# Kernel tuning notes

Measured on AMD Instinct MI355X. Metric: run time of the kernel, lower is better.

The kernel has to match this reference:

```python
import jax, jax.numpy as jnp
import numpy as np

N = 50000
IN_C = 128
HID = 128  # 2 * out_channels
OUT_C = 64
E = 800000


def setup_inputs() -> dict:
    key = jax.random.key(0)
    k1, k2, k3, k4, k5, k6 = jax.random.split(key, 6)
    x = jax.random.normal(k1, (N, IN_C), dtype=jnp.float32)
    edge_index = jax.random.randint(k2, (2, E), 0, N, dtype=jnp.int64)
    # Glorot init like PyG GCNConv
    W1 = jax.random.normal(k3, (IN_C, HID), dtype=jnp.float32) * np.sqrt(2.0 / (IN_C + HID))
    b1 = jnp.zeros((HID,), dtype=jnp.float32)
    W2 = jax.random.normal(k4, (HID, OUT_C), dtype=jnp.float32) * np.sqrt(2.0 / (HID + OUT_C))
    b2 = jnp.zeros((OUT_C,), dtype=jnp.float32)
    return {"x": x, "edge_index": edge_index, "W1": W1, "b1": b1, "W2": W2, "b2": b2}


def _gcn_norm(edge_index, num_nodes):
    # PyG gcn_norm with add_self_loops=True, edge_weight=1:
    # deg[i] = number of incoming edges to i (including self loop)
    # norm(e) = deg[src]^-0.5 * deg[dst]^-0.5
    loops = jnp.arange(num_nodes, dtype=edge_index.dtype)
    src = jnp.concatenate([edge_index[0], loops])
    dst = jnp.concatenate([edge_index[1], loops])
    deg = jax.ops.segment_sum(jnp.ones_like(dst, dtype=jnp.float32), dst,
                              num_segments=num_nodes)
    dinv = jnp.where(deg > 0, jax.lax.rsqrt(deg), 0.0)
    norm = dinv[src] * dinv[dst]
    return src, dst, norm


def _gcn_layer(x, W, b, src, dst, norm, num_nodes):
    h = x @ W                                    # [N, D_out] dense GEMM first (PyG order)
    msg = h[src] * norm[:, None]                 # gather + scale: [E+N, D_out]
    out = jax.ops.segment_sum(msg, dst, num_segments=num_nodes)  # scatter-add
    return out + b


def reference(x, edge_index, W1, b1, W2, b2):
    num_nodes = x.shape[0]
    # cached=True in the original: normalization computed once, reused by both convs
    src, dst, norm = _gcn_norm(edge_index, num_nodes)
    h = _gcn_layer(x, W1, b1, src, dst, norm, num_nodes)
    h = jax.nn.relu(h)
    out = _gcn_layer(h, W2, b2, src, dst, norm, num_nodes)
    return out
```

## Files before the change

### kernel.cpp

```cpp
#include <hip/hip_runtime.h>
#include <hip/hip_bf16.h>


typedef unsigned short ushort_t;
typedef __attribute__((ext_vector_type(8))) short bf16x8;
typedef __attribute__((ext_vector_type(4))) float f32x4;

__device__ __forceinline__ float blo(int v) {
    union { int i; float f; } u;
    u.i = v << 16;
    return u.f;
}

__device__ __forceinline__ float bhi(int v) {
    union { int i; float f; } u;
    u.i = v & 0xffff0000;
    return u.f;
}

__device__ __forceinline__ ushort_t f2bf(float f) {
    __hip_bfloat16 h = __float2bfloat16(f);
    return *reinterpret_cast<ushort_t*>(&h);
}

#define BMAX 512
#define CHUNK 2048
#define CAP 3072


__global__ __launch_bounds__(256) void gemm1bin_k(const float* __restrict__ X,
                                                  const float* __restrict__ W,
                                                  ushort_t* __restrict__ H,
                                                  const int* __restrict__ src,
                                                  const int* __restrict__ dst,
                                                  int* __restrict__ bucket_cursor,
                                                  int* __restrict__ binned,
                                                  int n, int E, int G1) {
    __shared__ __align__(16) char smem[52224];
    const int t = threadIdx.x;

    if ((int)blockIdx.x < G1) {
        ushort_t (*As)[136] = reinterpret_cast<ushort_t(*)[136]>(smem);
        ushort_t (*Bt)[136] = reinterpret_cast<ushort_t(*)[136]>(smem + 64 * 136 * 2);
        const int row0 = blockIdx.x * 64;
#pragma unroll
        for (int rep = 0; rep < 8; rep++) {
            int idx = rep * 1024 + t * 4;
            int r = idx >> 7, c = idx & 127;
            int gr = row0 + r;
            float4 v = make_float4(0.f, 0.f, 0.f, 0.f);
            if (gr < n) v = *reinterpret_cast<const float4*>(X + (size_t)gr * 128 + c);
            As[r][c + 0] = f2bf(v.x); As[r][c + 1] = f2bf(v.y);
            As[r][c + 2] = f2bf(v.z); As[r][c + 3] = f2bf(v.w);
        }
#pragma unroll
        for (int rep = 0; rep < 16; rep++) {
            int idx = rep * 1024 + t * 4;
            int k = idx >> 7, nn = idx & 127;
            float4 v = *reinterpret_cast<const float4*>(W + k * 128 + nn);
            Bt[nn + 0][k] = f2bf(v.x); Bt[nn + 1][k] = f2bf(v.y);
            Bt[nn + 2][k] = f2bf(v.z); Bt[nn + 3][k] = f2bf(v.w);
        }
        __syncthreads();
        const int lane = t & 63;
        const int wave = t >> 6;
        const int l15 = lane & 15;
        const int koff = (lane >> 4) * 8;
        f32x4 acc[8] = {};
#pragma unroll
        for (int ks = 0; ks < 4; ks++) {
            int kb = ks * 32 + koff;
            bf16x8 a = *reinterpret_cast<const bf16x8*>(&As[wave * 16 + l15][kb]);
#pragma unroll
            for (int tc = 0; tc < 8; tc++) {
                bf16x8 b = *reinterpret_cast<const bf16x8*>(&Bt[tc * 16 + l15][kb]);
                acc[tc] = __builtin_amdgcn_mfma_f32_16x16x32_bf16(a, b, acc[tc], 0, 0, 0);
            }
        }
        const int rbase = row0 + wave * 16 + (lane >> 4) * 4;
#pragma unroll
        for (int reg = 0; reg < 4; reg++) {
            int gr = rbase + reg;
            if (gr < n) {
#pragma unroll
                for (int tc = 0; tc < 8; tc++)
                    H[(size_t)gr * 128 + tc * 16 + l15] = f2bf(acc[tc][reg]);
            }
        }
    } else {
        int* lcnt = (int*)smem;
        int* lbase = lcnt + BMAX;
        int* lcur = lbase + BMAX;
        const int nchunks = (E + CHUNK - 1) / CHUNK;
        const int nbin = (int)gridDim.x - G1;
        for (int ch = (int)blockIdx.x - G1; ch < nchunks; ch += nbin) {
            int base = ch * CHUNK;
            int cnt = min(CHUNK, E - base);
            for (int i = t; i < BMAX; i += 256) lcnt[i] = 0;
            __syncthreads();
            for (int k = t; k < cnt; k += 256)
                atomicAdd(&lcnt[dst[base + k] >> 7], 1);
            __syncthreads();
            for (int i = t; i < BMAX; i += 256) {
                int c = lcnt[i];
                if (c) lbase[i] = atomicAdd(&bucket_cursor[i], c);
                lcur[i] = 0;
            }
            __syncthreads();
            for (int k = t; k < cnt; k += 256) {
                int d = dst[base + k];
                int b = d >> 7;
                int r = atomicAdd(&lcur[b], 1);
                int pos = lbase[b] + r;
                if (pos < CAP)
                    binned[b * CAP + pos] = (src[base + k] << 7) | (d & 127);
            }
            __syncthreads();
        }
    }
}

__global__ __launch_bounds__(256) void finalize_k(const int* __restrict__ binned,
                                                  const int* __restrict__ bucket_cursor,
                                                  float* __restrict__ dinv,
                                                  int2* __restrict__ row_range,
                                                  ushort_t* __restrict__ csr,
                                                  int N, int B) {
    __shared__ int dcnt[128];
    __shared__ int ebase[128];
    __shared__ int sc[128];
    int b = blockIdx.x;
    int tid = threadIdx.x;
    int node0 = b << 7;
    int nn = min(128, N - node0);
    int e0 = b * CAP;
    int e1 = e0 + min(bucket_cursor[b], CAP);

    if (tid < 128) dcnt[tid] = 0;
    __syncthreads();
    for (int k = e0 + tid; k < e1; k += 256)
        atomicAdd(&dcnt[binned[k] & 127], 1);
    __syncthreads();
    if (tid < 128) sc[tid] = (tid < nn) ? dcnt[tid] : 0;
    __syncthreads();
    for (int off = 1; off < 128; off <<= 1) {
        int t = 0;
        if (tid < 128 && tid >= off) t = sc[tid - off];
        __syncthreads();
        if (tid < 128) sc[tid] += t;
        __syncthreads();
    }
    if (tid < nn) {
        int deg = dcnt[tid];
        int ex = sc[tid] - deg;
        ebase[tid] = ex;
        int g = node0 + tid;
        dinv[g] = rsqrtf((float)deg + 1.0f);
        row_range[g] = make_int2(e0 + ex, e0 + ex + deg);
        dcnt[tid] = 0;
    }
    __syncthreads();
    const int t1 = N / 3, t2 = 2 * (N / 3);
#pragma unroll
    for (int ph = 0; ph < 3; ph++) {
        int lo = (ph == 0) ? 0 : (ph == 1 ? t1 : t2);
        int hi = (ph == 0) ? t1 : (ph == 1 ? t2 : N);
        for (int k = e0 + tid; k < e1; k += 256) {
            int e = binned[k];
            int s = (int)((unsigned)e >> 7);
            if (s >= lo && s < hi) {
                int low = e & 127;
                int r = atomicAdd(&dcnt[low], 1);
                csr[e0 + ebase[low] + r] = (ushort_t)s;
            }
        }
        __syncthreads();
    }
}


__global__ __launch_bounds__(256) void gemm2_k(const ushort_t* __restrict__ X,
                                               const float* __restrict__ W,
                                               const float* __restrict__ dinv,
                                               ushort_t* __restrict__ H, int n) {
    __shared__ ushort_t As[64][136];
    __shared__ ushort_t Bt[64][136];
    const int t = threadIdx.x;
    const int row0 = blockIdx.x * 64;
#pragma unroll
    for (int rep = 0; rep < 8; rep++) {
        int idx = rep * 1024 + t * 4;
        int r = idx >> 7, c = idx & 127;
        int gr = row0 + r;
        ushort4 v = make_ushort4(0, 0, 0, 0);
        if (gr < n) v = *reinterpret_cast<const ushort4*>(X + (size_t)gr * 128 + c);
        As[r][c + 0] = v.x; As[r][c + 1] = v.y; As[r][c + 2] = v.z; As[r][c + 3] = v.w;
    }
#pragma unroll
    for (int rep = 0; rep < 8; rep++) {
        int idx = rep * 1024 + t * 4;
        int k = idx >> 6, nn = idx & 63;
        float4 v = *reinterpret_cast<const float4*>(W + k * 64 + nn);
        Bt[nn + 0][k] = f2bf(v.x); Bt[nn + 1][k] = f2bf(v.y);
        Bt[nn + 2][k] = f2bf(v.z); Bt[nn + 3][k] = f2bf(v.w);
    }
    __syncthreads();
    const int lane = t & 63;
    const int wave = t >> 6;
    const int l15 = lane & 15;
    const int koff = (lane >> 4) * 8;
    f32x4 acc[4] = {};
#pragma unroll
    for (int ks = 0; ks < 4; ks++) {
        int kb = ks * 32 + koff;
        bf16x8 a = *reinterpret_cast<const bf16x8*>(&As[wave * 16 + l15][kb]);
#pragma unroll
        for (int tc = 0; tc < 4; tc++) {
            bf16x8 b = *reinterpret_cast<const bf16x8*>(&Bt[tc * 16 + l15][kb]);
            acc[tc] = __builtin_amdgcn_mfma_f32_16x16x32_bf16(a, b, acc[tc], 0, 0, 0);
        }
    }
    const int rbase = row0 + wave * 16 + (lane >> 4) * 4;
#pragma unroll
    for (int reg = 0; reg < 4; reg++) {
        int gr = rbase + reg;
        if (gr < n) {
            float dv = dinv[gr];
#pragma unroll
            for (int tc = 0; tc < 4; tc++)
                H[(size_t)gr * 64 + tc * 16 + l15] = f2bf(acc[tc][reg] * dv);
        }
    }
}

#define FMA8(VV, WT)                                                    \
    a0 = fmaf(blo((VV).x), (WT), a0); a1 = fmaf(bhi((VV).x), (WT), a1); \
    a2 = fmaf(blo((VV).y), (WT), a2); a3 = fmaf(bhi((VV).y), (WT), a3); \
    a4 = fmaf(blo((VV).z), (WT), a4); a5 = fmaf(bhi((VV).z), (WT), a5); \
    a6 = fmaf(blo((VV).w), (WT), a6); a7 = fmaf(bhi((VV).w), (WT), a7);


__global__ __launch_bounds__(256) void agg1_k(const ushort_t* __restrict__ h,
                                              const int2* __restrict__ row_range,
                                              const ushort_t* __restrict__ csr,
                                              const float* __restrict__ dinv,
                                              const float* __restrict__ bias,
                                              ushort_t* __restrict__ out, int n) {
    const int t = threadIdx.x;
    const int i = blockIdx.x * 16 + (t >> 4);
    if (i >= n) return;
    const int q = t & 15;
    const ushort_t* hq = h + 8 * q;
    float a0 = 0.f, a1 = 0.f, a2 = 0.f, a3 = 0.f;
    float a4 = 0.f, a5 = 0.f, a6 = 0.f, a7 = 0.f;
    const int2 rr = row_range[i];
    const int e = rr.y - 1;
    for (int j = rr.x; j < rr.y; j += 8) {
#pragma unroll
        for (int k = 0; k < 8; k++) {
            int jk = min(j + k, e);
            int s = (int)csr[jk];
            float w = (j + k <= e) ? dinv[s] : 0.f;
            int4 v = *reinterpret_cast<const int4*>(hq + (size_t)s * 128);
            FMA8(v, w);
        }
    }
    const float di = dinv[i];
    int4 sv = *reinterpret_cast<const int4*>(hq + (size_t)i * 128);
    FMA8(sv, di);
    float4 b0 = *reinterpret_cast<const float4*>(bias + 8 * q);
    float4 b1v = *reinterpret_cast<const float4*>(bias + 8 * q + 4);
    int4 o;
    o.x = (int)(((unsigned)f2bf(fmaxf(fmaf(di, a1, b0.y), 0.f)) << 16) | f2bf(fmaxf(fmaf(di, a0, b0.x), 0.f)));
    o.y = (int)(((unsigned)f2bf(fmaxf(fmaf(di, a3, b0.w), 0.f)) << 16) | f2bf(fmaxf(fmaf(di, a2, b0.z), 0.f)));
    o.z = (int)(((unsigned)f2bf(fmaxf(fmaf(di, a5, b1v.y), 0.f)) << 16) | f2bf(fmaxf(fmaf(di, a4, b1v.x), 0.f)));
    o.w = (int)(((unsigned)f2bf(fmaxf(fmaf(di, a7, b1v.w), 0.f)) << 16) | f2bf(fmaxf(fmaf(di, a6, b1v.z), 0.f)));
    *reinterpret_cast<int4*>(out + (size_t)i * 128 + 8 * q) = o;
}


__global__ __launch_bounds__(256) void agg2_k(const ushort_t* __restrict__ h,
                                              const int2* __restrict__ row_range,
                                              const ushort_t* __restrict__ csr,
                                              const float* __restrict__ dinv,
                                              const float* __restrict__ bias,
                                              float* __restrict__ out, int n) {
    const int t = threadIdx.x;
    const int i = blockIdx.x * 32 + (t >> 3);
    if (i >= n) return;
    const int q = t & 7;
    const ushort_t* hq = h + 8 * q;
    float a0 = 0.f, a1 = 0.f, a2 = 0.f, a3 = 0.f;
    float a4 = 0.f, a5 = 0.f, a6 = 0.f, a7 = 0.f;
    const int2 rr = row_range[i];
    const int e = rr.y - 1;
    for (int j = rr.x; j < rr.y; j += 8) {
#pragma unroll
        for (int k = 0; k < 8; k++) {
            int jk = min(j + k, e);
            int s = (int)csr[jk];
            float w = (j + k <= e) ? 1.f : 0.f;
            int4 v = *reinterpret_cast<const int4*>(hq + (size_t)s * 64);
            FMA8(v, w);
        }
    }
    int4 sv = *reinterpret_cast<const int4*>(hq + (size_t)i * 64);
    FMA8(sv, 1.f);
    const float di = dinv[i];
    float4 b0 = *reinterpret_cast<const float4*>(bias + 8 * q);
    float4 b1v = *reinterpret_cast<const float4*>(bias + 8 * q + 4);
    float4 o0 = make_float4(fmaf(di, a0, b0.x), fmaf(di, a1, b0.y),
                            fmaf(di, a2, b0.z), fmaf(di, a3, b0.w));
    float4 o1 = make_float4(fmaf(di, a4, b1v.x), fmaf(di, a5, b1v.y),
                            fmaf(di, a6, b1v.z), fmaf(di, a7, b1v.w));
    *reinterpret_cast<float4*>(out + (size_t)i * 64 + 8 * q) = o0;
    *reinterpret_cast<float4*>(out + (size_t)i * 64 + 8 * q + 4) = o1;
}


extern "C" void kernel_launch(void* const* d_in, const int* in_sizes, int n_in,
                              void* d_out, int out_size, void* d_ws, size_t ws_size,
                              hipStream_t stream) {
    const float* x   = (const float*)d_in[0];
    const int*   ei  = (const int*)d_in[1];
    const float* W1  = (const float*)d_in[2];
    const float* b1  = (const float*)d_in[3];
    const float* W2  = (const float*)d_in[4];
    const float* b2  = (const float*)d_in[5];
    float* out = (float*)d_out;

    const int N = in_sizes[0] / 128;
    const int E = in_sizes[1] / 2;
    const int B = (N + 127) >> 7;
    const int* src = ei;
    const int* dst = ei + E;

    char* p = (char*)d_ws;
    auto alloc = [&](size_t bytes) {
        char* q = p;
        p += (bytes + 255) & ~(size_t)255;
        return (void*)q;
    };
    int*      bucket_cursor = (int*)alloc((size_t)BMAX * 4);
    float*    dinv          = (float*)alloc((size_t)N * 4);
    int2*     row_range     = (int2*)alloc((size_t)N * 8);
    int*      binned        = (int*)alloc((size_t)B * CAP * 4);
    ushort_t* csr           = (ushort_t*)alloc(((size_t)B * CAP + 32) * 2);
    ushort_t* h1            = (ushort_t*)alloc((size_t)N * 128 * 2);
    ushort_t* agg1          = (ushort_t*)alloc((size_t)N * 128 * 2);
    ushort_t* h2            = h1;

    const int nchunks = (E + CHUNK - 1) / CHUNK;
    const int G1 = (N + 63) / 64;

    (void)hipMemsetAsync(bucket_cursor, 0, (size_t)B * 4, stream);
    gemm1bin_k<<<G1 + nchunks, 256, 0, stream>>>(x, W1, h1, src, dst,
                                                 bucket_cursor, binned, N, E, G1);
    finalize_k<<<B, 256, 0, stream>>>(binned, bucket_cursor, dinv, row_range, csr, N, B);

    agg1_k<<<(N + 15) / 16, 256, 0, stream>>>(h1, row_range, csr, dinv, b1, agg1, N);

    gemm2_k<<<(N + 63) / 64, 256, 0, stream>>>(agg1, W2, dinv, h2, N);
    agg2_k<<<(N + 31) / 32, 256, 0, stream>>>(h2, row_range, csr, dinv, b2, out, N);
}
```

Measured before the change: 185.4 us.

## Fuse layer-1 aggregation with layer-2 GEMM and split CSR fill into more phases

Layer-1 aggregation now writes its ReLU'd bf16 rows for each block of 16 nodes into shared memory, and the same block multiplies them by W2 with MFMA. This removes the separate gemm2 kernel and the global round trip of the N×128 intermediate. The cost is that every block re-converts all of W2 into shared memory, and the larger shared-memory footprint may lower occupancy. The finalize kernel's source-range phases go from 3 to 8, which changes the CSR fill ordering and locality but adds more passes over the binned edges.

```diff
diff --git a/kernel.cpp b/kernel.cpp
--- a/kernel.cpp
+++ b/kernel.cpp
@@ -26,6 +26,7 @@
 #define BMAX 512
 #define CHUNK 2048
 #define CAP 3072
+#define NPH 8
 
 
 __global__ __launch_bounds__(256) void gemm1bin_k(const float* __restrict__ X,
@@ -160,11 +161,10 @@
         dcnt[tid] = 0;
     }
     __syncthreads();
-    const int t1 = N / 3, t2 = 2 * (N / 3);
-#pragma unroll
-    for (int ph = 0; ph < 3; ph++) {
-        int lo = (ph == 0) ? 0 : (ph == 1 ? t1 : t2);
-        int hi = (ph == 0) ? t1 : (ph == 1 ? t2 : N);
+#pragma unroll
+    for (int ph = 0; ph < NPH; ph++) {
+        int lo = (int)((long long)N * ph / NPH);
+        int hi = (int)((long long)N * (ph + 1) / NPH);
         for (int k = e0 + tid; k < e1; k += 256) {
             int e = binned[k];
             int s = (int)((unsigned)e >> 7);
@@ -178,61 +178,6 @@
     }
 }
 
-
-__global__ __launch_bounds__(256) void gemm2_k(const ushort_t* __restrict__ X,
-                                               const float* __restrict__ W,
-                                               const float* __restrict__ dinv,
-                                               ushort_t* __restrict__ H, int n) {
-    __shared__ ushort_t As[64][136];
-    __shared__ ushort_t Bt[64][136];
-    const int t = threadIdx.x;
-    const int row0 = blockIdx.x * 64;
-#pragma unroll
-    for (int rep = 0; rep < 8; rep++) {
-        int idx = rep * 1024 + t * 4;
-        int r = idx >> 7, c = idx & 127;
-        int gr = row0 + r;
-        ushort4 v = make_ushort4(0, 0, 0, 0);
-        if (gr < n) v = *reinterpret_cast<const ushort4*>(X + (size_t)gr * 128 + c);
-        As[r][c + 0] = v.x; As[r][c + 1] = v.y; As[r][c + 2] = v.z; As[r][c + 3] = v.w;
-    }
-#pragma unroll
-    for (int rep = 0; rep < 8; rep++) {
-        int idx = rep * 1024 + t * 4;
-        int k = idx >> 6, nn = idx & 63;
-        float4 v = *reinterpret_cast<const float4*>(W + k * 64 + nn);
-        Bt[nn + 0][k] = f2bf(v.x); Bt[nn + 1][k] = f2bf(v.y);
-        Bt[nn + 2][k] = f2bf(v.z); Bt[nn + 3][k] = f2bf(v.w);
-    }
-    __syncthreads();
-    const int lane = t & 63;
-    const int wave = t >> 6;
-    const int l15 = lane & 15;
-    const int koff = (lane >> 4) * 8;
-    f32x4 acc[4] = {};
-#pragma unroll
-    for (int ks = 0; ks < 4; ks++) {
-        int kb = ks * 32 + koff;
-        bf16x8 a = *reinterpret_cast<const bf16x8*>(&As[wave * 16 + l15][kb]);
-#pragma unroll
-        for (int tc = 0; tc < 4; tc++) {
-            bf16x8 b = *reinterpret_cast<const bf16x8*>(&Bt[tc * 16 + l15][kb]);
-            acc[tc] = __builtin_amdgcn_mfma_f32_16x16x32_bf16(a, b, acc[tc], 0, 0, 0);
-        }
-    }
-    const int rbase = row0 + wave * 16 + (lane >> 4) * 4;
-#pragma unroll
-    for (int reg = 0; reg < 4; reg++) {
-        int gr = rbase + reg;
-        if (gr < n) {
-            float dv = dinv[gr];
-#pragma unroll
-            for (int tc = 0; tc < 4; tc++)
-                H[(size_t)gr * 64 + tc * 16 + l15] = f2bf(acc[tc][reg] * dv);
-        }
-    }
-}
-
 #define FMA8(VV, WT)                                                    \
     a0 = fmaf(blo((VV).x), (WT), a0); a1 = fmaf(bhi((VV).x), (WT), a1); \
     a2 = fmaf(blo((VV).y), (WT), a2); a3 = fmaf(bhi((VV).y), (WT), a3); \
@@ -240,44 +185,82 @@
     a6 = fmaf(blo((VV).w), (WT), a6); a7 = fmaf(bhi((VV).w), (WT), a7);
 
 
-__global__ __launch_bounds__(256) void agg1_k(const ushort_t* __restrict__ h,
-                                              const int2* __restrict__ row_range,
-                                              const ushort_t* __restrict__ csr,
-                                              const float* __restrict__ dinv,
-                                              const float* __restrict__ bias,
-                                              ushort_t* __restrict__ out, int n) {
+__global__ __launch_bounds__(256) void agg1mm2_k(const ushort_t* __restrict__ h,
+                                                 const int2* __restrict__ row_range,
+                                                 const ushort_t* __restrict__ csr,
+                                                 const float* __restrict__ dinv,
+                                                 const float* __restrict__ b1,
+                                                 const float* __restrict__ W2,
+                                                 ushort_t* __restrict__ h2,
+                                                 int n) {
+    __shared__ ushort_t As[16][136];
+    __shared__ ushort_t Bt[64][136];
     const int t = threadIdx.x;
-    const int i = blockIdx.x * 16 + (t >> 4);
-    if (i >= n) return;
+    const int row0 = blockIdx.x * 16;
+
+#pragma unroll
+    for (int rep = 0; rep < 8; rep++) {
+        int idx = rep * 1024 + t * 4;
+        int k = idx >> 6, c = idx & 63;
+        float4 v = *reinterpret_cast<const float4*>(W2 + k * 64 + c);
+        Bt[c + 0][k] = f2bf(v.x); Bt[c + 1][k] = f2bf(v.y);
+        Bt[c + 2][k] = f2bf(v.z); Bt[c + 3][k] = f2bf(v.w);
+    }
+
+    const int i = row0 + (t >> 4);
     const int q = t & 15;
-    const ushort_t* hq = h + 8 * q;
-    float a0 = 0.f, a1 = 0.f, a2 = 0.f, a3 = 0.f;
-    float a4 = 0.f, a5 = 0.f, a6 = 0.f, a7 = 0.f;
-    const int2 rr = row_range[i];
-    const int e = rr.y - 1;
-    for (int j = rr.x; j < rr.y; j += 8) {
-#pragma unroll
-        for (int k = 0; k < 8; k++) {
-            int jk = min(j + k, e);
-            int s = (int)csr[jk];
-            float w = (j + k <= e) ? dinv[s] : 0.f;
-            int4 v = *reinterpret_cast<const int4*>(hq + (size_t)s * 128);
-            FMA8(v, w);
-        }
-    }
-    const float di = dinv[i];
-    int4 sv = *reinterpret_cast<const int4*>(hq + (size_t)i * 128);
-    FMA8(sv, di);
-    float4 b0 = *reinterpret_cast<const float4*>(bias + 8 * q);
-    float4 b1v = *reinterpret_cast<const float4*>(bias + 8 * q + 4);
-    int4 o;
-    o.x = (int)(((unsigned)f2bf(fmaxf(fmaf(di, a1, b0.y), 0.f)) << 16) | f2bf(fmaxf(fmaf(di, a0, b0.x), 0.f)));
-    o.y = (int)(((unsigned)f2bf(fmaxf(fmaf(di, a3, b0.w), 0.f)) << 16) | f2bf(fmaxf(fmaf(di, a2, b0.z), 0.f)));
-    o.z = (int)(((unsigned)f2bf(fmaxf(fmaf(di, a5, b1v.y), 0.f)) << 16) | f2bf(fmaxf(fmaf(di, a4, b1v.x), 0.f)));
-    o.w = (int)(((unsigned)f2bf(fmaxf(fmaf(di, a7, b1v.w), 0.f)) << 16) | f2bf(fmaxf(fmaf(di, a6, b1v.z), 0.f)));
-    *reinterpret_cast<int4*>(out + (size_t)i * 128 + 8 * q) = o;
-}
-
+    if (i < n) {
+        const ushort_t* hq = h + 8 * q;
+        float a0 = 0.f, a1 = 0.f, a2 = 0.f, a3 = 0.f;
+        float a4 = 0.f, a5 = 0.f, a6 = 0.f, a7 = 0.f;
+        const int2 rr = row_range[i];
+        const int e = rr.y - 1;
+        for (int j = rr.x; j < rr.y; j += 8) {
+#pragma unroll
+            for (int k = 0; k < 8; k++) {
+                int jk = min(j + k, e);
+                int s = (int)csr[jk];
+                float w = (j + k <= e) ? dinv[s] : 0.f;
+                int4 v = *reinterpret_cast<const int4*>(hq + (size_t)s * 128);
+                FMA8(v, w);
+            }
+        }
+        const float di = dinv[i];
+        int4 sv = *reinterpret_cast<const int4*>(hq + (size_t)i * 128);
+        FMA8(sv, di);
+        float4 c0 = *reinterpret_cast<const float4*>(b1 + 8 * q);
+        float4 c1 = *reinterpret_cast<const float4*>(b1 + 8 * q + 4);
+        int4 o;
+        o.x = (int)(((unsigned)f2bf(fmaxf(fmaf(di, a1, c0.y), 0.f)) << 16) | f2bf(fmaxf(fmaf(di, a0, c0.x), 0.f)));
+        o.y = (int)(((unsigned)f2bf(fmaxf(fmaf(di, a3, c0.w), 0.f)) << 16) | f2bf(fmaxf(fmaf(di, a2, c0.z), 0.f)));
+        o.z = (int)(((unsigned)f2bf(fmaxf(fmaf(di, a5, c1.y), 0.f)) << 16) | f2bf(fmaxf(fmaf(di, a4, c1.x), 0.f)));
+        o.w = (int)(((unsigned)f2bf(fmaxf(fmaf(di, a7, c1.w), 0.f)) << 16) | f2bf(fmaxf(fmaf(di, a6, c1.z), 0.f)));
+        *reinterpret_cast<int4*>(&As[t >> 4][8 * q]) = o;
+    }
+    __syncthreads();
+
+    const int lane = t & 63;
+    const int wave = t >> 6;
+    const int l15 = lane & 15;
+    const int koff = (lane >> 4) * 8;
+    f32x4 acc = {};
+#pragma unroll
+    for (int ks = 0; ks < 4; ks++) {
+        int kb = ks * 32 + koff;
+        bf16x8 a = *reinterpret_cast<const bf16x8*>(&As[l15][kb]);
+        bf16x8 b = *reinterpret_cast<const bf16x8*>(&Bt[wave * 16 + l15][kb]);
+        acc = __builtin_amdgcn_mfma_f32_16x16x32_bf16(a, b, acc, 0, 0, 0);
+    }
+#pragma unroll
+    for (int reg = 0; reg < 4; reg++) {
+        int gr = row0 + (lane >> 4) * 4 + reg;
+        if (gr < n)
+            h2[(size_t)gr * 64 + wave * 16 + l15] = f2bf(acc[reg] * dinv[gr]);
+    }
+}
+
+
+#define ADDW8(VV, WT) FMA8(VV, WT)
 
 __global__ __launch_bounds__(256) void agg2_k(const ushort_t* __restrict__ h,
                                               const int2* __restrict__ row_range,
@@ -347,8 +330,7 @@
     int*      binned        = (int*)alloc((size_t)B * CAP * 4);
     ushort_t* csr           = (ushort_t*)alloc(((size_t)B * CAP + 32) * 2);
     ushort_t* h1            = (ushort_t*)alloc((size_t)N * 128 * 2);
-    ushort_t* agg1          = (ushort_t*)alloc((size_t)N * 128 * 2);
-    ushort_t* h2            = h1;
+    ushort_t* h2            = (ushort_t*)alloc((size_t)N * 64 * 2);
 
     const int nchunks = (E + CHUNK - 1) / CHUNK;
     const int G1 = (N + 63) / 64;
@@ -358,8 +340,7 @@
                                                  bucket_cursor, binned, N, E, G1);
     finalize_k<<<B, 256, 0, stream>>>(binned, bucket_cursor, dinv, row_range, csr, N, B);
 
-    agg1_k<<<(N + 15) / 16, 256, 0, stream>>>(h1, row_range, csr, dinv, b1, agg1, N);
-
-    gemm2_k<<<(N + 63) / 64, 256, 0, stream>>>(agg1, W2, dinv, h2, N);
+    agg1mm2_k<<<(N + 15) / 16, 256, 0, stream>>>(h1, row_range, csr, dinv, b1, W2, h2, N);
+
     agg2_k<<<(N + 31) / 32, 256, 0, stream>>>(h2, row_range, csr, dinv, b2, out, N);
 }
```

New measurement: 201.0 us. +8.4%, slower.

## Single-pass CSR fill with 8-way source phases; unroll aggregation gathers to 16

Applied to the files above, without the earlier changes.

The finalize kernel now counts each destination's edges per source-range phase (8 phases) in one pass. It prefix-sums those counts and scatters every edge in one more pass. This replaces the earlier three filtered passes over the binned edges and still sorts sources coarsely by range for gather locality. Both aggregation kernels now load 16 neighbor indices and weights up front before issuing the row gathers, so more memory loads are in flight at once. The cost is higher register use and more padded iterations for low-degree nodes.

```diff
diff --git a/kernel.cpp b/kernel.cpp
--- a/kernel.cpp
+++ b/kernel.cpp
@@ -26,6 +26,7 @@
 #define BMAX 512
 #define CHUNK 2048
 #define CAP 3072
+#define NPH 8
 
 
 __global__ __launch_bounds__(256) void gemm1bin_k(const float* __restrict__ X,
@@ -126,8 +127,7 @@
                                                   int2* __restrict__ row_range,
                                                   ushort_t* __restrict__ csr,
                                                   int N, int B) {
-    __shared__ int dcnt[128];
-    __shared__ int ebase[128];
+    __shared__ int cnt[128][NPH];
     __shared__ int sc[128];
     int b = blockIdx.x;
     int tid = threadIdx.x;
@@ -135,46 +135,45 @@
     int nn = min(128, N - node0);
     int e0 = b * CAP;
     int e1 = e0 + min(bucket_cursor[b], CAP);
-
-    if (tid < 128) dcnt[tid] = 0;
-    __syncthreads();
-    for (int k = e0 + tid; k < e1; k += 256)
-        atomicAdd(&dcnt[binned[k] & 127], 1);
-    __syncthreads();
-    if (tid < 128) sc[tid] = (tid < nn) ? dcnt[tid] : 0;
+    const int phw = (N + NPH - 1) / NPH;
+
+    for (int i = tid; i < 128 * NPH; i += 256) ((int*)cnt)[i] = 0;
+    __syncthreads();
+    for (int k = e0 + tid; k < e1; k += 256) {
+        int e = binned[k];
+        int s = (int)((unsigned)e >> 7);
+        atomicAdd(&cnt[e & 127][s / phw], 1);
+    }
+    __syncthreads();
+    int deg = 0;
+    int pre[NPH];
+    if (tid < 128) {
+#pragma unroll
+        for (int p = 0; p < NPH; p++) { pre[p] = deg; deg += cnt[tid][p]; }
+        sc[tid] = (tid < nn) ? deg : 0;
+    }
     __syncthreads();
     for (int off = 1; off < 128; off <<= 1) {
-        int t = 0;
-        if (tid < 128 && tid >= off) t = sc[tid - off];
+        int t2 = 0;
+        if (tid < 128 && tid >= off) t2 = sc[tid - off];
         __syncthreads();
-        if (tid < 128) sc[tid] += t;
+        if (tid < 128) sc[tid] += t2;
         __syncthreads();
     }
     if (tid < nn) {
-        int deg = dcnt[tid];
         int ex = sc[tid] - deg;
-        ebase[tid] = ex;
         int g = node0 + tid;
         dinv[g] = rsqrtf((float)deg + 1.0f);
         row_range[g] = make_int2(e0 + ex, e0 + ex + deg);
-        dcnt[tid] = 0;
-    }
-    __syncthreads();
-    const int t1 = N / 3, t2 = 2 * (N / 3);
-#pragma unroll
-    for (int ph = 0; ph < 3; ph++) {
-        int lo = (ph == 0) ? 0 : (ph == 1 ? t1 : t2);
-        int hi = (ph == 0) ? t1 : (ph == 1 ? t2 : N);
-        for (int k = e0 + tid; k < e1; k += 256) {
-            int e = binned[k];
-            int s = (int)((unsigned)e >> 7);
-            if (s >= lo && s < hi) {
-                int low = e & 127;
-                int r = atomicAdd(&dcnt[low], 1);
-                csr[e0 + ebase[low] + r] = (ushort_t)s;
-            }
-        }
-        __syncthreads();
+#pragma unroll
+        for (int p = 0; p < NPH; p++) cnt[tid][p] = ex + pre[p];
+    }
+    __syncthreads();
+    for (int k = e0 + tid; k < e1; k += 256) {
+        int e = binned[k];
+        int s = (int)((unsigned)e >> 7);
+        int slot = atomicAdd(&cnt[e & 127][s / phw], 1);
+        csr[e0 + slot] = (ushort_t)s;
     }
 }
 
@@ -255,14 +254,17 @@
     float a4 = 0.f, a5 = 0.f, a6 = 0.f, a7 = 0.f;
     const int2 rr = row_range[i];
     const int e = rr.y - 1;
-    for (int j = rr.x; j < rr.y; j += 8) {
-#pragma unroll
-        for (int k = 0; k < 8; k++) {
-            int jk = min(j + k, e);
-            int s = (int)csr[jk];
-            float w = (j + k <= e) ? dinv[s] : 0.f;
-            int4 v = *reinterpret_cast<const int4*>(hq + (size_t)s * 128);
-            FMA8(v, w);
+    for (int j = rr.x; j < rr.y; j += 16) {
+        int ss[16];
+#pragma unroll
+        for (int k = 0; k < 16; k++) ss[k] = (int)csr[min(j + k, e)];
+        float ww[16];
+#pragma unroll
+        for (int k = 0; k < 16; k++) ww[k] = (j + k <= e) ? dinv[ss[k]] : 0.f;
+#pragma unroll
+        for (int k = 0; k < 16; k++) {
+            int4 v = *reinterpret_cast<const int4*>(hq + (size_t)ss[k] * 128);
+            FMA8(v, ww[k]);
         }
     }
     const float di = dinv[i];
@@ -294,14 +296,17 @@
     float a4 = 0.f, a5 = 0.f, a6 = 0.f, a7 = 0.f;
     const int2 rr = row_range[i];
     const int e = rr.y - 1;
-    for (int j = rr.x; j < rr.y; j += 8) {
-#pragma unroll
-        for (int k = 0; k < 8; k++) {
-            int jk = min(j + k, e);
-            int s = (int)csr[jk];
-            float w = (j + k <= e) ? 1.f : 0.f;
-            int4 v = *reinterpret_cast<const int4*>(hq + (size_t)s * 64);
-            FMA8(v, w);
+    for (int j = rr.x; j < rr.y; j += 16) {
+        int ss[16];
+#pragma unroll
+        for (int k = 0; k < 16; k++) ss[k] = (int)csr[min(j + k, e)];
+        float ww[16];
+#pragma unroll
+        for (int k = 0; k < 16; k++) ww[k] = (j + k <= e) ? 1.f : 0.f;
+#pragma unroll
+        for (int k = 0; k < 16; k++) {
+            int4 v = *reinterpret_cast<const int4*>(hq + (size_t)ss[k] * 64);
+            FMA8(v, ww[k]);
         }
     }
     int4 sv = *reinterpret_cast<const int4*>(hq + (size_t)i * 64);
```

Result: no change. 185.6 us (+0.1%).
